# Kernel optimization log

Measured on AMD Instinct MI355X. Metric: run time of the kernel, lower is better.

## Reference

```python
import jax, jax.numpy as jnp
import numpy as np

B, T, I, H, L = 32, 1024, 1024, 1024, 3


def setup_inputs() -> dict:
    key = jax.random.key(0)
    ks = jax.random.split(key, 8)
    sc_in = 1.0 / np.sqrt(I)
    sc_h = 1.0 / np.sqrt(H)
    return {
        "x": jax.random.normal(ks[0], (B, T, I), dtype=jnp.float32),
        "s0": jnp.zeros((B, H), dtype=jnp.float32),
        "w_h": jax.random.normal(ks[1], (I, H), dtype=jnp.float32) * sc_in,
        "w_t": jax.random.normal(ks[2], (I, H), dtype=jnp.float32) * sc_in,
        "w_c": jax.random.normal(ks[3], (I, H), dtype=jnp.float32) * sc_in,
        "Rh": jax.random.normal(ks[4], (L, H, H), dtype=jnp.float32) * sc_h,
        "Rt": jax.random.normal(ks[5], (L, H, H), dtype=jnp.float32) * sc_h,
        "Rc": jax.random.normal(ks[6], (L, H, H), dtype=jnp.float32) * sc_h,
        "bh": jnp.zeros((L, H), dtype=jnp.float32),
        "bt": jnp.zeros((L, H), dtype=jnp.float32),
        "bc": jnp.zeros((L, H), dtype=jnp.float32),
    }


def reference(x, s0, w_h, w_t, w_c, Rh, Rt, Rc, bh, bt, bc):
    # x: [B, T, I]; s0: [B, H]. Dropout prob = 0 -> identity.
    num_layers = Rh.shape[0]

    def step(s, x_t):
        # Input projections only feed layer 0 (as in the torch code).
        whx = x_t @ w_h  # [B, H]
        wtx = x_t @ w_t
        wcx = x_t @ w_c
        for l in range(num_layers):
            h_in = (whx if l == 0 else 0.0) + s @ Rh[l].T + bh[l]
            t_in = (wtx if l == 0 else 0.0) + s @ Rt[l].T + bt[l]
            c_in = (wcx if l == 0 else 0.0) + s @ Rc[l].T + bc[l]
            h = jnp.tanh(h_in)
            t = jax.nn.sigmoid(t_in)
            c = jax.nn.sigmoid(c_in)
            s = h * t + s * c
        return s, s

    x_tbi = jnp.swapaxes(x, 0, 1)  # [T, B, I] for scan over time
    s_T, outs = jax.lax.scan(step, s0, x_tbi)
    return jnp.swapaxes(outs, 0, 1), s_T  # ([B, T, H], [B, H])
```

## Files before the change

### kernel.cpp

```cpp
#include <hip/hip_runtime.h>
#include <hip/hip_bf16.h>

static constexpr int Bb = 32;
static constexpr int Tt = 1024;
static constexpr int Ii = 1024;
static constexpr int Hh = 1024;
static constexpr int NWG = 256;

static constexpr int SLOT_E = Hh * Bb;
static constexpr int NSLOT  = 3 * Tt + 1;

typedef float f4 __attribute__((ext_vector_type(4)));

static constexpr int LDS_WORDS = 36 * 1024 + 2 * 1536;
static constexpr int LDS_BYTES = LDS_WORDS * 4;

static constexpr unsigned SENT32 = 0x7FC0DEADu;
static constexpr unsigned SENT16 = 0x7FC1u;

template <typename PT> __device__ __forceinline__ float pt_to_f(PT v);
template <> __device__ __forceinline__ float pt_to_f<float>(float v) { return v; }
template <> __device__ __forceinline__ float pt_to_f<__hip_bfloat16>(__hip_bfloat16 v) { return __bfloat162float(v); }

template <typename PT> __device__ __forceinline__ PT f_to_pt(float v);
template <> __device__ __forceinline__ float f_to_pt<float>(float v) { return v; }
template <> __device__ __forceinline__ __hip_bfloat16 f_to_pt<__hip_bfloat16>(float v) { return __float2bfloat16(v); }

#define BGLD(dst, p, lit) \
    asm volatile("global_load_dwordx4 %0, %1, off offset:" lit " sc0 sc1" : "=v"(dst) : "v"(p))
#define BG8(sv, p, a,b,c,d2,e,f,g2,h) \
    BGLD(sv[0],p,a); BGLD(sv[1],p,b); BGLD(sv[2],p,c); BGLD(sv[3],p,d2); \
    BGLD(sv[4],p,e); BGLD(sv[5],p,f); BGLD(sv[6],p,g2); BGLD(sv[7],p,h)
#define BGLD2(dst, p, lit) \
    asm volatile("global_load_dwordx2 %0, %1, off offset:" lit " sc0 sc1" : "=v"(dst) : "v"(p))
#define BG8x2(su, p, a,b,c,d2,e,f,g2,h) \
    BGLD2(su[0],p,a); BGLD2(su[1],p,b); BGLD2(su[2],p,c); BGLD2(su[3],p,d2); \
    BGLD2(su[4],p,e); BGLD2(su[5],p,f); BGLD2(su[6],p,g2); BGLD2(su[7],p,h)
#define VWAIT(n) do { asm volatile("s_waitcnt vmcnt(" #n ")" ::: "memory"); \
                      __builtin_amdgcn_sched_barrier(0); } while (0)

__device__ __forceinline__ int grp_ok32(const f4* sv) {
    int ok = 1;
#pragma unroll
    for (int i = 0; i < 8; ++i)
#pragma unroll
        for (int j = 0; j < 4; ++j)
            ok &= (__float_as_uint(sv[i][j]) != SENT32);
    return ok;
}
__device__ __forceinline__ int grp_ok16(const uint2* su) {
    int ok = 1;
#pragma unroll
    for (int i = 0; i < 8; ++i) {
        ok &= ((su[i].x & 0xFFFFu) != SENT16) & ((su[i].x >> 16) != SENT16);
        ok &= ((su[i].y & 0xFFFFu) != SENT16) & ((su[i].y >> 16) != SENT16);
    }
    return ok;
}

template <typename PT>
__global__ __launch_bounds__(256, 2) void proj_gemm(
    const float* __restrict__ X, const float* __restrict__ Wh,
    const float* __restrict__ Wt, const float* __restrict__ Wc,
    PT* __restrict__ P2)
{
    __shared__ float smem[4160];
    float* As = smem;
    float* Bs = smem + 1088;

    const int tid = threadIdx.x;
    const int tx = tid & 15, ty = tid >> 4;
    const int col0 = blockIdx.x * 64;
    const int t0 = blockIdx.y * 2;

    float acc[3][4][4];
#pragma unroll
    for (int g = 0; g < 3; ++g)
#pragma unroll
        for (int mm = 0; mm < 4; ++mm)
#pragma unroll
            for (int nn = 0; nn < 4; ++nn) acc[g][mm][nn] = 0.f;

    const int lm = tid >> 2, lk4 = (tid & 3) * 4;
    const float* aptr = X + ((size_t)(lm & 31) * Tt + (t0 + (lm >> 5))) * Ii + lk4;
    const int bk = tid >> 4, bn4 = (tid & 15) * 4;

    for (int k0 = 0; k0 < Ii; k0 += 16) {
        float4 av = *(const float4*)(aptr + k0);
        As[(lk4 + 0) * 68 + lm] = av.x;
        As[(lk4 + 1) * 68 + lm] = av.y;
        As[(lk4 + 2) * 68 + lm] = av.z;
        As[(lk4 + 3) * 68 + lm] = av.w;
        *(float4*)&Bs[0 * 1024 + bk * 64 + bn4] = *(const float4*)(Wh + (size_t)(k0 + bk) * Hh + col0 + bn4);
        *(float4*)&Bs[1 * 1024 + bk * 64 + bn4] = *(const float4*)(Wt + (size_t)(k0 + bk) * Hh + col0 + bn4);
        *(float4*)&Bs[2 * 1024 + bk * 64 + bn4] = *(const float4*)(Wc + (size_t)(k0 + bk) * Hh + col0 + bn4);
        __syncthreads();
#pragma unroll
        for (int k = 0; k < 16; ++k) {
            float4 a = *(const float4*)&As[k * 68 + ty * 4];
            float a_[4] = {a.x, a.y, a.z, a.w};
#pragma unroll
            for (int g = 0; g < 3; ++g) {
                float4 b = *(const float4*)&Bs[g * 1024 + k * 64 + tx * 4];
                float b_[4] = {b.x, b.y, b.z, b.w};
#pragma unroll
                for (int mm = 0; mm < 4; ++mm)
#pragma unroll
                    for (int nn = 0; nn < 4; ++nn)
                        acc[g][mm][nn] += a_[mm] * b_[nn];
            }
        }
        __syncthreads();
    }

    float* E = smem;
    const int b4 = (tid & 7) * 4;
#pragma unroll 1
    for (int g = 0; g < 3; ++g) {
        __syncthreads();
#pragma unroll
        for (int mm = 0; mm < 4; ++mm)
#pragma unroll
            for (int nn = 0; nn < 4; ++nn)
                E[(ty * 4 + mm) * 65 + tx * 4 + nn] = acc[g][mm][nn];
        __syncthreads();
        PT* dst = P2 + (size_t)g * Tt * Hh * Bb;
#pragma unroll
        for (int it = 0; it < 4; ++it) {
            const int line = (tid >> 3) + it * 32;
            const int tt = line >> 6, hh = line & 63;
            const float o0 = E[(tt * 32 + b4 + 0) * 65 + hh];
            const float o1 = E[(tt * 32 + b4 + 1) * 65 + hh];
            const float o2v = E[(tt * 32 + b4 + 2) * 65 + hh];
            const float o3 = E[(tt * 32 + b4 + 3) * 65 + hh];
            PT* d = dst + ((size_t)(t0 + tt) * Hh + col0 + hh) * Bb + b4;
            d[0] = f_to_pt<PT>(o0); d[1] = f_to_pt<PT>(o1);
            d[2] = f_to_pt<PT>(o2v); d[3] = f_to_pt<PT>(o3);
        }
    }
}

template <typename RT>
__global__ __launch_bounds__(256) void init_ring(const float* __restrict__ s0,
                                                 RT* __restrict__ ring)
{
    const size_t tid = (size_t)blockIdx.x * 256 + threadIdx.x;
    if (tid < (size_t)Bb * Hh) {
        const int b = (int)(tid >> 10), h = (int)(tid & 1023);
        ring[h * 32 + b] = f_to_pt<RT>(s0[tid]);
    }
    const unsigned sw = (sizeof(RT) == 4) ? SENT32 : ((SENT16 << 16) | SENT16);
    const uint4 pat = {sw, sw, sw, sw};
    uint4* base = (uint4*)(ring + SLOT_E);
    const size_t n16 = (size_t)(NSLOT - 1) * SLOT_E * sizeof(RT) / 16;
    const size_t stride = (size_t)gridDim.x * 256;
    for (size_t i = tid; i < n16; i += stride) base[i] = pat;
}

template <typename RT>
__global__ __launch_bounds__(256) void out_transpose(
    const RT* __restrict__ ring, float* __restrict__ out, float* __restrict__ sT)
{
    __shared__ float tile[128 * 33];
    const int tid = threadIdx.x;
    const int h0 = blockIdx.x * 128;
    const int t = blockIdx.y;
    const RT* src = ring + (size_t)(3 * t + 3) * SLOT_E + h0 * 32;
#pragma unroll
    for (int e = 0; e < 16; ++e) {
        const int idx = e * 256 + tid;
        tile[(idx >> 5) * 33 + (idx & 31)] = pt_to_f<RT>(src[idx]);
    }
    __syncthreads();
    const int hi = tid & 31, bq = tid >> 5;
#pragma unroll
    for (int e = 0; e < 4; ++e) {
        const int b = bq + e * 8;
        float4 v;
        v.x = tile[(hi * 4 + 0) * 33 + b];
        v.y = tile[(hi * 4 + 1) * 33 + b];
        v.z = tile[(hi * 4 + 2) * 33 + b];
        v.w = tile[(hi * 4 + 3) * 33 + b];
        *(float4*)(out + ((size_t)b * Tt + t) * Hh + h0 + hi * 4) = v;
        if (t == Tt - 1) *(float4*)(sT + (size_t)b * Hh + h0 + hi * 4) = v;
    }
}

template <typename PT, typename RT>
__global__ __launch_bounds__(256, 1) void rhn_recur(
    const float* __restrict__ Rh, const float* __restrict__ Rt,
    const float* __restrict__ Rc, const float* __restrict__ bh,
    const float* __restrict__ bt, const float* __restrict__ bc,
    const PT* __restrict__ P2, RT* __restrict__ ring)
{
    extern __shared__ float lds[];

    const int g = blockIdx.x;
    const int tid = threadIdx.x;

    {
        const int k4 = tid * 4;
        const int sk = k4 ^ (((k4 >> 5) & 7) << 2);
#pragma unroll 1
        for (int j = 0; j < 36; ++j) {
            const int l = j / 12;
            const int rem = j - l * 12;
            const int gt = rem >> 2;
            const int q = rem & 3;
            const int h = (q << 8) | g;
            const float* src = (gt == 0 ? Rh : (gt == 1 ? Rt : Rc)) + ((size_t)l * Hh + h) * Hh;
            *(float4*)&lds[(j << 10) | sk] = *(const float4*)(src + k4);
        }
    }
    __syncthreads();

    const int ks = tid >> 3;
    const int b0 = (tid & 7) << 2;
    const int q8 = ks & 7;
    const int wv = tid >> 6;
    const int ub = tid & 31;
    const int uqc = (tid >> 5) & 3;
    const int uhc = (uqc << 8) | g;

    int o2[8];
#pragma unroll
    for (int c = 0; c < 8; ++c) o2[c] = ((c ^ q8) << 2);

    float brh[3], brt[3], brc[3];
#pragma unroll
    for (int l = 0; l < 3; ++l) {
        brh[l] = bh[l * Hh + uhc];
        brt[l] = bt[l * Hh + uhc];
        brc[l] = bc[l * Hh + uhc];
    }

    float so_reg = pt_to_f<RT>(ring[uhc * 32 + ub]);

#pragma unroll 1
    for (int t = 0; t < Tt; ++t) {
#pragma unroll 1
        for (int l = 0; l < 3; ++l) {
            const int p = t * 3 + l;
            float* part = lds + 36 * 1024 + (p & 1) * 1536;

            float pv0 = 0.f, pv1 = 0.f, pv2 = 0.f;
            if (l == 0 && tid < 128) {
                const size_t pb = ((size_t)t * Hh + uhc) * Bb + ub;
                pv0 = pt_to_f<PT>(P2[pb]);
                pv1 = pt_to_f<PT>(P2[(size_t)Tt * Hh * Bb + pb]);
                pv2 = pt_to_f<PT>(P2[2 * (size_t)Tt * Hh * Bb + pb]);
            }

            const float* rp = lds + l * 12288 + (ks << 5);

            f4 accv[12];
#pragma unroll
            for (int jj = 0; jj < 12; ++jj) accv[jj] = (f4){0.f, 0.f, 0.f, 0.f};

            if constexpr (sizeof(RT) == 4) {
                const float* sA = (const float*)ring + (size_t)p * SLOT_E + (ks << 5) * 32 + b0;
                f4 sv0[8], sv1[8];
                BG8(sv0, sA, "0","128","256","384","512","640","768","896");
                BG8(sv1, sA, "1024","1152","1280","1408","1536","1664","1792","1920");
                VWAIT(8);
                while (!__all(grp_ok32(sv0))) {
                    __builtin_amdgcn_s_sleep(1);
                    BG8(sv0, sA, "0","128","256","384","512","640","768","896");
                    VWAIT(0);
                }
#pragma unroll
                for (int jj = 0; jj < 12; ++jj) {
                    const f4 r0 = *(const f4*)(rp + jj * 1024 + o2[0]);
                    const f4 r1 = *(const f4*)(rp + jj * 1024 + o2[1]);
                    f4 a = accv[jj];
                    a += sv0[0] * r0[0]; a += sv0[1] * r0[1]; a += sv0[2] * r0[2]; a += sv0[3] * r0[3];
                    a += sv0[4] * r1[0]; a += sv0[5] * r1[1]; a += sv0[6] * r1[2]; a += sv0[7] * r1[3];
                    accv[jj] = a;
                }
                BG8(sv0, sA, "2048","2176","2304","2432","2560","2688","2816","2944");
                VWAIT(8);
                while (!__all(grp_ok32(sv1))) {
                    __builtin_amdgcn_s_sleep(1);
                    BG8(sv1, sA, "1024","1152","1280","1408","1536","1664","1792","1920");
                    VWAIT(0);
                }
#pragma unroll
                for (int jj = 0; jj < 12; ++jj) {
                    const f4 r0 = *(const f4*)(rp + jj * 1024 + o2[2]);
                    const f4 r1 = *(const f4*)(rp + jj * 1024 + o2[3]);
                    f4 a = accv[jj];
                    a += sv1[0] * r0[0]; a += sv1[1] * r0[1]; a += sv1[2] * r0[2]; a += sv1[3] * r0[3];
                    a += sv1[4] * r1[0]; a += sv1[5] * r1[1]; a += sv1[6] * r1[2]; a += sv1[7] * r1[3];
                    accv[jj] = a;
                }
                BG8(sv1, sA, "3072","3200","3328","3456","3584","3712","3840","3968");
                VWAIT(8);
                while (!__all(grp_ok32(sv0))) {
                    __builtin_amdgcn_s_sleep(1);
                    BG8(sv0, sA, "2048","2176","2304","2432","2560","2688","2816","2944");
                    VWAIT(0);
                }
#pragma unroll
                for (int jj = 0; jj < 12; ++jj) {
                    const f4 r0 = *(const f4*)(rp + jj * 1024 + o2[4]);
                    const f4 r1 = *(const f4*)(rp + jj * 1024 + o2[5]);
                    f4 a = accv[jj];
                    a += sv0[0] * r0[0]; a += sv0[1] * r0[1]; a += sv0[2] * r0[2]; a += sv0[3] * r0[3];
                    a += sv0[4] * r1[0]; a += sv0[5] * r1[1]; a += sv0[6] * r1[2]; a += sv0[7] * r1[3];
                    accv[jj] = a;
                }
                VWAIT(0);
                while (!__all(grp_ok32(sv1))) {
                    __builtin_amdgcn_s_sleep(1);
                    BG8(sv1, sA, "3072","3200","3328","3456","3584","3712","3840","3968");
                    VWAIT(0);
                }
#pragma unroll
                for (int jj = 0; jj < 12; ++jj) {
                    const f4 r0 = *(const f4*)(rp + jj * 1024 + o2[6]);
                    const f4 r1 = *(const f4*)(rp + jj * 1024 + o2[7]);
                    f4 a = accv[jj];
                    a += sv1[0] * r0[0]; a += sv1[1] * r0[1]; a += sv1[2] * r0[2]; a += sv1[3] * r0[3];
                    a += sv1[4] * r1[0]; a += sv1[5] * r1[1]; a += sv1[6] * r1[2]; a += sv1[7] * r1[3];
                    accv[jj] = a;
                }
            } else {
                const __hip_bfloat16* sIn = (const __hip_bfloat16*)ring + (size_t)p * SLOT_E + (ks << 5) * 32 + b0;
#pragma unroll 1
                for (int blk = 0; blk < 4; ++blk) {
                    uint2 su[8];
                    const __hip_bfloat16* pb2 = sIn + (size_t)blk * 256;
                    BG8x2(su, pb2, "0","64","128","192","256","320","384","448");
                    VWAIT(0);
                    while (!__all(grp_ok16(su))) {
                        __builtin_amdgcn_s_sleep(1);
                        BG8x2(su, pb2, "0","64","128","192","256","320","384","448");
                        VWAIT(0);
                    }
                    f4 sv[8];
#pragma unroll
                    for (int i = 0; i < 8; ++i) {
                        sv[i][0] = __uint_as_float(su[i].x << 16);
                        sv[i][1] = __uint_as_float(su[i].x & 0xFFFF0000u);
                        sv[i][2] = __uint_as_float(su[i].y << 16);
                        sv[i][3] = __uint_as_float(su[i].y & 0xFFFF0000u);
                    }
#pragma unroll
                    for (int jj = 0; jj < 12; ++jj) {
                        const f4 r0 = *(const f4*)(rp + jj * 1024 + o2[blk * 2]);
                        const f4 r1 = *(const f4*)(rp + jj * 1024 + o2[blk * 2 + 1]);
                        f4 a = accv[jj];
                        a += sv[0] * r0[0]; a += sv[1] * r0[1]; a += sv[2] * r0[2]; a += sv[3] * r0[3];
                        a += sv[4] * r1[0]; a += sv[5] * r1[1]; a += sv[6] * r1[2]; a += sv[7] * r1[3];
                        accv[jj] = a;
                    }
                }
            }

#pragma unroll
            for (int jj = 0; jj < 12; ++jj) {
#pragma unroll
                for (int st = 8; st <= 32; st <<= 1) {
                    accv[jj][0] += __shfl_xor(accv[jj][0], st);
                    accv[jj][1] += __shfl_xor(accv[jj][1], st);
                    accv[jj][2] += __shfl_xor(accv[jj][2], st);
                    accv[jj][3] += __shfl_xor(accv[jj][3], st);
                }
            }
            f4 s1 = accv[0];
#pragma unroll
            for (int j2 = 1; j2 < 8; ++j2) if (q8 == j2) s1 = accv[j2];
            f4 s2 = accv[8];
#pragma unroll
            for (int j2 = 1; j2 < 4; ++j2) if (q8 == j2) s2 = accv[8 + j2];
            *(f4*)&part[(wv * 12 + q8) * 32 + b0] = s1;
            if (q8 < 4) *(f4*)&part[(wv * 12 + 8 + q8) * 32 + b0] = s2;
            __syncthreads();

            if (tid < 128) {
                float vals[3];
#pragma unroll
                for (int gt = 0; gt < 3; ++gt) {
                    const int jl = (gt << 2) + uqc;
                    vals[gt] = part[jl * 32 + ub] + part[(12 + jl) * 32 + ub]
                             + part[(24 + jl) * 32 + ub] + part[(36 + jl) * 32 + ub];
                }
                float bb0, bb1, bb2;
                if (l == 0)      { bb0 = brh[0]; bb1 = brt[0]; bb2 = brc[0]; }
                else if (l == 1) { bb0 = brh[1]; bb1 = brt[1]; bb2 = brc[1]; }
                else             { bb0 = brh[2]; bb1 = brt[2]; bb2 = brc[2]; }
                vals[0] += bb0; vals[1] += bb1; vals[2] += bb2;
                if (l == 0) { vals[0] += pv0; vals[1] += pv1; vals[2] += pv2; }
                const float hv = 1.f - 2.f / (1.f + __expf(2.f * vals[0]));
                const float tv = 1.f / (1.f + __expf(-vals[1]));
                const float cv = 1.f / (1.f + __expf(-vals[2]));
                const float sn = hv * tv + so_reg * cv;
                so_reg = sn;
                RT* wp = ring + (size_t)(p + 1) * SLOT_E + uhc * 32 + ub;
                if constexpr (sizeof(RT) == 4) {
                    __hip_atomic_store((float*)wp, sn, __ATOMIC_RELAXED, __HIP_MEMORY_SCOPE_AGENT);
                } else {
                    __hip_bfloat16 b16 = __float2bfloat16(sn);
                    __hip_atomic_store((unsigned short*)wp, *(unsigned short*)&b16,
                                       __ATOMIC_RELAXED, __HIP_MEMORY_SCOPE_AGENT);
                }
            }
        }
    }
}

extern "C" void kernel_launch(void* const* d_in, const int* in_sizes, int n_in,
                              void* d_out, int out_size, void* d_ws, size_t ws_size,
                              hipStream_t stream)
{
    (void)in_sizes; (void)n_in; (void)out_size;
    const float* x  = (const float*)d_in[0];
    const float* s0 = (const float*)d_in[1];
    const float* wh = (const float*)d_in[2];
    const float* wt = (const float*)d_in[3];
    const float* wc = (const float*)d_in[4];
    const float* Rh = (const float*)d_in[5];
    const float* Rt = (const float*)d_in[6];
    const float* Rc = (const float*)d_in[7];
    const float* bh = (const float*)d_in[8];
    const float* bt = (const float*)d_in[9];
    const float* bc = (const float*)d_in[10];

    float* out = (float*)d_out;
    float* sT  = out + (size_t)Bb * Tt * Hh;

    const size_t THB  = (size_t)Tt * Hh * Bb;
    const size_t p2f  = 3 * THB * 4, p2h = 3 * THB * 2;
    const size_t ringF = (size_t)NSLOT * SLOT_E * 4;
    const size_t ringH = (size_t)NSLOT * SLOT_E * 2;

    char* w = (char*)d_ws;

    if (ws_size >= p2f + ringF) {
        float* P2 = (float*)w;
        float* ring = (float*)(w + p2f);
        proj_gemm<float><<<dim3(16, 512), 256, 0, stream>>>(x, wh, wt, wc, P2);
        init_ring<float><<<2048, 256, 0, stream>>>(s0, ring);
        hipFuncSetAttribute(reinterpret_cast<const void*>(rhn_recur<float, float>),
                            hipFuncAttributeMaxDynamicSharedMemorySize, LDS_BYTES);
        void* args[] = {(void*)&Rh, (void*)&Rt, (void*)&Rc, (void*)&bh, (void*)&bt, (void*)&bc,
                        (void*)&P2, (void*)&ring};
        hipLaunchCooperativeKernel(reinterpret_cast<void*>(rhn_recur<float, float>),
                                   dim3(NWG), dim3(256), args, LDS_BYTES, stream);
        out_transpose<float><<<dim3(8, 1024), 256, 0, stream>>>(ring, out, sT);
    } else if (ws_size >= p2h + ringF) {
        __hip_bfloat16* P2 = (__hip_bfloat16*)w;
        float* ring = (float*)(w + p2h);
        proj_gemm<__hip_bfloat16><<<dim3(16, 512), 256, 0, stream>>>(x, wh, wt, wc, P2);
        init_ring<float><<<2048, 256, 0, stream>>>(s0, ring);
        hipFuncSetAttribute(reinterpret_cast<const void*>(rhn_recur<__hip_bfloat16, float>),
                            hipFuncAttributeMaxDynamicSharedMemorySize, LDS_BYTES);
        void* args[] = {(void*)&Rh, (void*)&Rt, (void*)&Rc, (void*)&bh, (void*)&bt, (void*)&bc,
                        (void*)&P2, (void*)&ring};
        hipLaunchCooperativeKernel(reinterpret_cast<void*>(rhn_recur<__hip_bfloat16, float>),
                                   dim3(NWG), dim3(256), args, LDS_BYTES, stream);
        out_transpose<float><<<dim3(8, 1024), 256, 0, stream>>>(ring, out, sT);
    } else {
        __hip_bfloat16* P2 = (__hip_bfloat16*)w;
        __hip_bfloat16* ring = (__hip_bfloat16*)(w + p2h);
        proj_gemm<__hip_bfloat16><<<dim3(16, 512), 256, 0, stream>>>(x, wh, wt, wc, P2);
        init_ring<__hip_bfloat16><<<2048, 256, 0, stream>>>(s0, ring);
        hipFuncSetAttribute(reinterpret_cast<const void*>(rhn_recur<__hip_bfloat16, __hip_bfloat16>),
                            hipFuncAttributeMaxDynamicSharedMemorySize, LDS_BYTES);
        void* args[] = {(void*)&Rh, (void*)&Rt, (void*)&Rc, (void*)&bh, (void*)&bt, (void*)&bc,
                        (void*)&P2, (void*)&ring};
        hipLaunchCooperativeKernel(reinterpret_cast<void*>(rhn_recur<__hip_bfloat16, __hip_bfloat16>),
                                   dim3(NWG), dim3(256), args, LDS_BYTES, stream);
        out_transpose<__hip_bfloat16><<<dim3(8, 1024), 256, 0, stream>>>(ring, out, sT);
    }
}
```

Baseline: 32.00 ms.

## Replace full-length sentinel ring with 16-slot tagged ring and history buffer

```diff
diff --git a/kernel.cpp b/kernel.cpp
--- a/kernel.cpp
+++ b/kernel.cpp
@@ -8,15 +8,12 @@
 static constexpr int NWG = 256;
 
 static constexpr int SLOT_E = Hh * Bb;
-static constexpr int NSLOT  = 3 * Tt + 1;
+static constexpr int NS     = 16;
 
 typedef float f4 __attribute__((ext_vector_type(4)));
 
 static constexpr int LDS_WORDS = 36 * 1024 + 2 * 1536;
 static constexpr int LDS_BYTES = LDS_WORDS * 4;
-
-static constexpr unsigned SENT32 = 0x7FC0DEADu;
-static constexpr unsigned SENT16 = 0x7FC1u;
 
 template <typename PT> __device__ __forceinline__ float pt_to_f(PT v);
 template <> __device__ __forceinline__ float pt_to_f<float>(float v) { return v; }
@@ -25,38 +22,40 @@
 template <typename PT> __device__ __forceinline__ PT f_to_pt(float v);
 template <> __device__ __forceinline__ float f_to_pt<float>(float v) { return v; }
 template <> __device__ __forceinline__ __hip_bfloat16 f_to_pt<__hip_bfloat16>(float v) { return __float2bfloat16(v); }
+
+__device__ __forceinline__ void backoff(int it) {
+    if (it < 2)      __builtin_amdgcn_s_sleep(1);
+    else if (it < 4) __builtin_amdgcn_s_sleep(2);
+    else if (it < 8) __builtin_amdgcn_s_sleep(4);
+    else             __builtin_amdgcn_s_sleep(8);
+}
 
 #define BGLD(dst, p, lit) \
     asm volatile("global_load_dwordx4 %0, %1, off offset:" lit " sc0 sc1" : "=v"(dst) : "v"(p))
 #define BG8(sv, p, a,b,c,d2,e,f,g2,h) \
     BGLD(sv[0],p,a); BGLD(sv[1],p,b); BGLD(sv[2],p,c); BGLD(sv[3],p,d2); \
     BGLD(sv[4],p,e); BGLD(sv[5],p,f); BGLD(sv[6],p,g2); BGLD(sv[7],p,h)
-#define BGLD2(dst, p, lit) \
-    asm volatile("global_load_dwordx2 %0, %1, off offset:" lit " sc0 sc1" : "=v"(dst) : "v"(p))
-#define BG8x2(su, p, a,b,c,d2,e,f,g2,h) \
-    BGLD2(su[0],p,a); BGLD2(su[1],p,b); BGLD2(su[2],p,c); BGLD2(su[3],p,d2); \
-    BGLD2(su[4],p,e); BGLD2(su[5],p,f); BGLD2(su[6],p,g2); BGLD2(su[7],p,h)
 #define VWAIT(n) do { asm volatile("s_waitcnt vmcnt(" #n ")" ::: "memory"); \
                       __builtin_amdgcn_sched_barrier(0); } while (0)
 
-__device__ __forceinline__ int grp_ok32(const f4* sv) {
+__device__ __forceinline__ int grp_tag32(const f4* sv, unsigned texp) {
     int ok = 1;
 #pragma unroll
     for (int i = 0; i < 8; ++i)
 #pragma unroll
         for (int j = 0; j < 4; ++j)
-            ok &= (__float_as_uint(sv[i][j]) != SENT32);
+            ok &= (int)((__float_as_uint(sv[i][j]) & 3u) == texp);
     return ok;
 }
-__device__ __forceinline__ int grp_ok16(const uint2* su) {
-    int ok = 1;
-#pragma unroll
-    for (int i = 0; i < 8; ++i) {
-        ok &= ((su[i].x & 0xFFFFu) != SENT16) & ((su[i].x >> 16) != SENT16);
-        ok &= ((su[i].y & 0xFFFFu) != SENT16) & ((su[i].y >> 16) != SENT16);
-    }
-    return ok;
-}
+
+#define RETRY32T(sv, texp, p, a,b,c,d2,e,f,g2,h) \
+    { int _it = 0; \
+      while (!__all(grp_tag32(sv, texp))) { \
+          if (_it) backoff(_it); \
+          ++_it; \
+          BG8(sv, p, a,b,c,d2,e,f,g2,h); \
+          VWAIT(0); \
+      } }
 
 template <typename PT>
 __global__ __launch_bounds__(256, 2) void proj_gemm(
@@ -140,36 +139,33 @@
     }
 }
 
-template <typename RT>
-__global__ __launch_bounds__(256) void init_ring(const float* __restrict__ s0,
-                                                 RT* __restrict__ ring)
+__global__ __launch_bounds__(256) void init_ring_s(const float* __restrict__ s0,
+                                                   float* __restrict__ ring)
 {
     const size_t tid = (size_t)blockIdx.x * 256 + threadIdx.x;
     if (tid < (size_t)Bb * Hh) {
         const int b = (int)(tid >> 10), h = (int)(tid & 1023);
-        ring[h * 32 + b] = f_to_pt<RT>(s0[tid]);
-    }
-    const unsigned sw = (sizeof(RT) == 4) ? SENT32 : ((SENT16 << 16) | SENT16);
-    const uint4 pat = {sw, sw, sw, sw};
+        ring[h * 32 + b] = __uint_as_float(__float_as_uint(s0[tid]) & ~3u);
+    }
+    const uint4 pat = {3u, 3u, 3u, 3u};
     uint4* base = (uint4*)(ring + SLOT_E);
-    const size_t n16 = (size_t)(NSLOT - 1) * SLOT_E * sizeof(RT) / 16;
+    const size_t n16 = (size_t)(NS - 1) * SLOT_E * 4 / 16;
     const size_t stride = (size_t)gridDim.x * 256;
     for (size_t i = tid; i < n16; i += stride) base[i] = pat;
 }
 
-template <typename RT>
-__global__ __launch_bounds__(256) void out_transpose(
-    const RT* __restrict__ ring, float* __restrict__ out, float* __restrict__ sT)
+__global__ __launch_bounds__(256) void out_transpose_hist(
+    const float* __restrict__ shist, float* __restrict__ out, float* __restrict__ sT)
 {
     __shared__ float tile[128 * 33];
     const int tid = threadIdx.x;
     const int h0 = blockIdx.x * 128;
     const int t = blockIdx.y;
-    const RT* src = ring + (size_t)(3 * t + 3) * SLOT_E + h0 * 32;
+    const float* src = shist + ((size_t)t * Hh + h0) * Bb;
 #pragma unroll
     for (int e = 0; e < 16; ++e) {
         const int idx = e * 256 + tid;
-        tile[(idx >> 5) * 33 + (idx & 31)] = pt_to_f<RT>(src[idx]);
+        tile[(idx >> 5) * 33 + (idx & 31)] = src[idx];
     }
     __syncthreads();
     const int hi = tid & 31, bq = tid >> 5;
@@ -186,12 +182,13 @@
     }
 }
 
-template <typename PT, typename RT>
+template <typename PT>
 __global__ __launch_bounds__(256, 1) void rhn_recur(
     const float* __restrict__ Rh, const float* __restrict__ Rt,
     const float* __restrict__ Rc, const float* __restrict__ bh,
     const float* __restrict__ bt, const float* __restrict__ bc,
-    const PT* __restrict__ P2, RT* __restrict__ ring)
+    const PT* __restrict__ P2, float* __restrict__ ring,
+    float* __restrict__ shist, const float* __restrict__ s0in)
 {
     extern __shared__ float lds[];
 
@@ -234,13 +231,17 @@
         brc[l] = bc[l * Hh + uhc];
     }
 
-    float so_reg = pt_to_f<RT>(ring[uhc * 32 + ub]);
+    float so_reg = (tid < 128) ? s0in[(size_t)ub * Hh + uhc] : 0.f;
 
 #pragma unroll 1
     for (int t = 0; t < Tt; ++t) {
 #pragma unroll 1
         for (int l = 0; l < 3; ++l) {
             const int p = t * 3 + l;
+            const int slr = p & (NS - 1);
+            const unsigned texp = (unsigned)((p >> 4) & 3);
+            const int slw = (p + 1) & (NS - 1);
+            const unsigned twr = (unsigned)(((p + 1) >> 4) & 3);
             float* part = lds + 36 * 1024 + (p & 1) * 1536;
 
             float pv0 = 0.f, pv1 = 0.f, pv2 = 0.f;
@@ -257,104 +258,55 @@
 #pragma unroll
             for (int jj = 0; jj < 12; ++jj) accv[jj] = (f4){0.f, 0.f, 0.f, 0.f};
 
-            if constexpr (sizeof(RT) == 4) {
-                const float* sA = (const float*)ring + (size_t)p * SLOT_E + (ks << 5) * 32 + b0;
-                f4 sv0[8], sv1[8];
-                BG8(sv0, sA, "0","128","256","384","512","640","768","896");
-                BG8(sv1, sA, "1024","1152","1280","1408","1536","1664","1792","1920");
-                VWAIT(8);
-                while (!__all(grp_ok32(sv0))) {
-                    __builtin_amdgcn_s_sleep(1);
-                    BG8(sv0, sA, "0","128","256","384","512","640","768","896");
-                    VWAIT(0);
-                }
-#pragma unroll
-                for (int jj = 0; jj < 12; ++jj) {
-                    const f4 r0 = *(const f4*)(rp + jj * 1024 + o2[0]);
-                    const f4 r1 = *(const f4*)(rp + jj * 1024 + o2[1]);
-                    f4 a = accv[jj];
-                    a += sv0[0] * r0[0]; a += sv0[1] * r0[1]; a += sv0[2] * r0[2]; a += sv0[3] * r0[3];
-                    a += sv0[4] * r1[0]; a += sv0[5] * r1[1]; a += sv0[6] * r1[2]; a += sv0[7] * r1[3];
-                    accv[jj] = a;
-                }
-                BG8(sv0, sA, "2048","2176","2304","2432","2560","2688","2816","2944");
-                VWAIT(8);
-                while (!__all(grp_ok32(sv1))) {
-                    __builtin_amdgcn_s_sleep(1);
-                    BG8(sv1, sA, "1024","1152","1280","1408","1536","1664","1792","1920");
-                    VWAIT(0);
-                }
-#pragma unroll
-                for (int jj = 0; jj < 12; ++jj) {
-                    const f4 r0 = *(const f4*)(rp + jj * 1024 + o2[2]);
-                    const f4 r1 = *(const f4*)(rp + jj * 1024 + o2[3]);
-                    f4 a = accv[jj];
-                    a += sv1[0] * r0[0]; a += sv1[1] * r0[1]; a += sv1[2] * r0[2]; a += sv1[3] * r0[3];
-                    a += sv1[4] * r1[0]; a += sv1[5] * r1[1]; a += sv1[6] * r1[2]; a += sv1[7] * r1[3];
-                    accv[jj] = a;
-                }
-                BG8(sv1, sA, "3072","3200","3328","3456","3584","3712","3840","3968");
-                VWAIT(8);
-                while (!__all(grp_ok32(sv0))) {
-                    __builtin_amdgcn_s_sleep(1);
-                    BG8(sv0, sA, "2048","2176","2304","2432","2560","2688","2816","2944");
-                    VWAIT(0);
-                }
-#pragma unroll
-                for (int jj = 0; jj < 12; ++jj) {
-                    const f4 r0 = *(const f4*)(rp + jj * 1024 + o2[4]);
-                    const f4 r1 = *(const f4*)(rp + jj * 1024 + o2[5]);
-                    f4 a = accv[jj];
-                    a += sv0[0] * r0[0]; a += sv0[1] * r0[1]; a += sv0[2] * r0[2]; a += sv0[3] * r0[3];
-                    a += sv0[4] * r1[0]; a += sv0[5] * r1[1]; a += sv0[6] * r1[2]; a += sv0[7] * r1[3];
-                    accv[jj] = a;
-                }
-                VWAIT(0);
-                while (!__all(grp_ok32(sv1))) {
-                    __builtin_amdgcn_s_sleep(1);
-                    BG8(sv1, sA, "3072","3200","3328","3456","3584","3712","3840","3968");
-                    VWAIT(0);
-                }
-#pragma unroll
-                for (int jj = 0; jj < 12; ++jj) {
-                    const f4 r0 = *(const f4*)(rp + jj * 1024 + o2[6]);
-                    const f4 r1 = *(const f4*)(rp + jj * 1024 + o2[7]);
-                    f4 a = accv[jj];
-                    a += sv1[0] * r0[0]; a += sv1[1] * r0[1]; a += sv1[2] * r0[2]; a += sv1[3] * r0[3];
-                    a += sv1[4] * r1[0]; a += sv1[5] * r1[1]; a += sv1[6] * r1[2]; a += sv1[7] * r1[3];
-                    accv[jj] = a;
-                }
-            } else {
-                const __hip_bfloat16* sIn = (const __hip_bfloat16*)ring + (size_t)p * SLOT_E + (ks << 5) * 32 + b0;
-#pragma unroll 1
-                for (int blk = 0; blk < 4; ++blk) {
-                    uint2 su[8];
-                    const __hip_bfloat16* pb2 = sIn + (size_t)blk * 256;
-                    BG8x2(su, pb2, "0","64","128","192","256","320","384","448");
-                    VWAIT(0);
-                    while (!__all(grp_ok16(su))) {
-                        __builtin_amdgcn_s_sleep(1);
-                        BG8x2(su, pb2, "0","64","128","192","256","320","384","448");
-                        VWAIT(0);
-                    }
-                    f4 sv[8];
-#pragma unroll
-                    for (int i = 0; i < 8; ++i) {
-                        sv[i][0] = __uint_as_float(su[i].x << 16);
-                        sv[i][1] = __uint_as_float(su[i].x & 0xFFFF0000u);
-                        sv[i][2] = __uint_as_float(su[i].y << 16);
-                        sv[i][3] = __uint_as_float(su[i].y & 0xFFFF0000u);
-                    }
-#pragma unroll
-                    for (int jj = 0; jj < 12; ++jj) {
-                        const f4 r0 = *(const f4*)(rp + jj * 1024 + o2[blk * 2]);
-                        const f4 r1 = *(const f4*)(rp + jj * 1024 + o2[blk * 2 + 1]);
-                        f4 a = accv[jj];
-                        a += sv[0] * r0[0]; a += sv[1] * r0[1]; a += sv[2] * r0[2]; a += sv[3] * r0[3];
-                        a += sv[4] * r1[0]; a += sv[5] * r1[1]; a += sv[6] * r1[2]; a += sv[7] * r1[3];
-                        accv[jj] = a;
-                    }
-                }
+            const float* sA = ring + (size_t)slr * SLOT_E + (ks << 5) * 32 + b0;
+            f4 sv0[8], sv1[8];
+            BG8(sv0, sA, "0","128","256","384","512","640","768","896");
+            BG8(sv1, sA, "1024","1152","1280","1408","1536","1664","1792","1920");
+            VWAIT(8);
+            RETRY32T(sv0, texp, sA, "0","128","256","384","512","640","768","896");
+#pragma unroll
+            for (int jj = 0; jj < 12; ++jj) {
+                const f4 r0 = *(const f4*)(rp + jj * 1024 + o2[0]);
+                const f4 r1 = *(const f4*)(rp + jj * 1024 + o2[1]);
+                f4 a = accv[jj];
+                a += sv0[0] * r0[0]; a += sv0[1] * r0[1]; a += sv0[2] * r0[2]; a += sv0[3] * r0[3];
+                a += sv0[4] * r1[0]; a += sv0[5] * r1[1]; a += sv0[6] * r1[2]; a += sv0[7] * r1[3];
+                accv[jj] = a;
+            }
+            BG8(sv0, sA, "2048","2176","2304","2432","2560","2688","2816","2944");
+            VWAIT(8);
+            RETRY32T(sv1, texp, sA, "1024","1152","1280","1408","1536","1664","1792","1920");
+#pragma unroll
+            for (int jj = 0; jj < 12; ++jj) {
+                const f4 r0 = *(const f4*)(rp + jj * 1024 + o2[2]);
+                const f4 r1 = *(const f4*)(rp + jj * 1024 + o2[3]);
+                f4 a = accv[jj];
+                a += sv1[0] * r0[0]; a += sv1[1] * r0[1]; a += sv1[2] * r0[2]; a += sv1[3] * r0[3];
+                a += sv1[4] * r1[0]; a += sv1[5] * r1[1]; a += sv1[6] * r1[2]; a += sv1[7] * r1[3];
+                accv[jj] = a;
+            }
+            BG8(sv1, sA, "3072","3200","3328","3456","3584","3712","3840","3968");
+            VWAIT(8);
+            RETRY32T(sv0, texp, sA, "2048","2176","2304","2432","2560","2688","2816","2944");
+#pragma unroll
+            for (int jj = 0; jj < 12; ++jj) {
+                const f4 r0 = *(const f4*)(rp + jj * 1024 + o2[4]);
+                const f4 r1 = *(const f4*)(rp + jj * 1024 + o2[5]);
+                f4 a = accv[jj];
+                a += sv0[0] * r0[0]; a += sv0[1] * r0[1]; a += sv0[2] * r0[2]; a += sv0[3] * r0[3];
+                a += sv0[4] * r1[0]; a += sv0[5] * r1[1]; a += sv0[6] * r1[2]; a += sv0[7] * r1[3];
+                accv[jj] = a;
+            }
+            VWAIT(0);
+            RETRY32T(sv1, texp, sA, "3072","3200","3328","3456","3584","3712","3840","3968");
+#pragma unroll
+            for (int jj = 0; jj < 12; ++jj) {
+                const f4 r0 = *(const f4*)(rp + jj * 1024 + o2[6]);
+                const f4 r1 = *(const f4*)(rp + jj * 1024 + o2[7]);
+                f4 a = accv[jj];
+                a += sv1[0] * r0[0]; a += sv1[1] * r0[1]; a += sv1[2] * r0[2]; a += sv1[3] * r0[3];
+                a += sv1[4] * r1[0]; a += sv1[5] * r1[1]; a += sv1[6] * r1[2]; a += sv1[7] * r1[3];
+                accv[jj] = a;
             }
 
 #pragma unroll
@@ -396,16 +348,31 @@
                 const float cv = 1.f / (1.f + __expf(-vals[2]));
                 const float sn = hv * tv + so_reg * cv;
                 so_reg = sn;
-                RT* wp = ring + (size_t)(p + 1) * SLOT_E + uhc * 32 + ub;
-                if constexpr (sizeof(RT) == 4) {
-                    __hip_atomic_store((float*)wp, sn, __ATOMIC_RELAXED, __HIP_MEMORY_SCOPE_AGENT);
-                } else {
-                    __hip_bfloat16 b16 = __float2bfloat16(sn);
-                    __hip_atomic_store((unsigned short*)wp, *(unsigned short*)&b16,
-                                       __ATOMIC_RELAXED, __HIP_MEMORY_SCOPE_AGENT);
-                }
+                const unsigned bits = (__float_as_uint(sn) & ~3u) | twr;
+                __hip_atomic_store((unsigned*)(ring + (size_t)slw * SLOT_E + uhc * 32 + ub),
+                                   bits, __ATOMIC_RELAXED, __HIP_MEMORY_SCOPE_AGENT);
+                if (l == 2)
+                    shist[((size_t)t * Hh + uhc) * Bb + ub] = sn;
             }
         }
+    }
+}
+
+template <typename PT>
+static void launch_recur(const float* Rh, const float* Rt, const float* Rc,
+                         const float* bh, const float* bt, const float* bc,
+                         const PT* P2, float* ring, float* shist,
+                         const float* s0, hipStream_t stream)
+{
+    (void)hipFuncSetAttribute(reinterpret_cast<const void*>(rhn_recur<PT>),
+                              hipFuncAttributeMaxDynamicSharedMemorySize, LDS_BYTES);
+    void* args[] = {(void*)&Rh, (void*)&Rt, (void*)&Rc, (void*)&bh, (void*)&bt, (void*)&bc,
+                    (void*)&P2, (void*)&ring, (void*)&shist, (void*)&s0};
+    hipError_t e = hipLaunchCooperativeKernel(reinterpret_cast<void*>(rhn_recur<PT>),
+                                              dim3(NWG), dim3(256), args, LDS_BYTES, stream);
+    if (e != hipSuccess) {
+        rhn_recur<PT><<<dim3(NWG), dim3(256), LDS_BYTES, stream>>>(
+            Rh, Rt, Rc, bh, bt, bc, P2, ring, shist, s0);
     }
 }
 
@@ -429,48 +396,28 @@
     float* out = (float*)d_out;
     float* sT  = out + (size_t)Bb * Tt * Hh;
 
-    const size_t THB  = (size_t)Tt * Hh * Bb;
-    const size_t p2f  = 3 * THB * 4, p2h = 3 * THB * 2;
-    const size_t ringF = (size_t)NSLOT * SLOT_E * 4;
-    const size_t ringH = (size_t)NSLOT * SLOT_E * 2;
+    const size_t THB   = (size_t)Tt * Hh * Bb;
+    const size_t p2f   = 3 * THB * 4, p2h = 3 * THB * 2;
+    const size_t ringS = (size_t)NS * SLOT_E * 4;
+    const size_t shF   = THB * 4;
 
     char* w = (char*)d_ws;
 
-    if (ws_size >= p2f + ringF) {
+    if (ws_size >= p2f + ringS + shF + 4096) {
         float* P2 = (float*)w;
         float* ring = (float*)(w + p2f);
+        float* shist = (float*)(w + p2f + ringS);
         proj_gemm<float><<<dim3(16, 512), 256, 0, stream>>>(x, wh, wt, wc, P2);
-        init_ring<float><<<2048, 256, 0, stream>>>(s0, ring);
-        hipFuncSetAttribute(reinterpret_cast<const void*>(rhn_recur<float, float>),
-                            hipFuncAttributeMaxDynamicSharedMemorySize, LDS_BYTES);
-        void* args[] = {(void*)&Rh, (void*)&Rt, (void*)&Rc, (void*)&bh, (void*)&bt, (void*)&bc,
-                        (void*)&P2, (void*)&ring};
-        hipLaunchCooperativeKernel(reinterpret_cast<void*>(rhn_recur<float, float>),
-                                   dim3(NWG), dim3(256), args, LDS_BYTES, stream);
-        out_transpose<float><<<dim3(8, 1024), 256, 0, stream>>>(ring, out, sT);
-    } else if (ws_size >= p2h + ringF) {
+        init_ring_s<<<128, 256, 0, stream>>>(s0, ring);
+        launch_recur<float>(Rh, Rt, Rc, bh, bt, bc, P2, ring, shist, s0, stream);
+        out_transpose_hist<<<dim3(8, 1024), 256, 0, stream>>>(shist, out, sT);
+    } else {
         __hip_bfloat16* P2 = (__hip_bfloat16*)w;
         float* ring = (float*)(w + p2h);
+        float* shist = (float*)(w + p2h + ringS);
         proj_gemm<__hip_bfloat16><<<dim3(16, 512), 256, 0, stream>>>(x, wh, wt, wc, P2);
-        init_ring<float><<<2048, 256, 0, stream>>>(s0, ring);
-        hipFuncSetAttribute(reinterpret_cast<const void*>(rhn_recur<__hip_bfloat16, float>),
-                            hipFuncAttributeMaxDynamicSharedMemorySize, LDS_BYTES);
-        void* args[] = {(void*)&Rh, (void*)&Rt, (void*)&Rc, (void*)&bh, (void*)&bt, (void*)&bc,
-                        (void*)&P2, (void*)&ring};
-        hipLaunchCooperativeKernel(reinterpret_cast<void*>(rhn_recur<__hip_bfloat16, float>),
-                                   dim3(NWG), dim3(256), args, LDS_BYTES, stream);
-        out_transpose<float><<<dim3(8, 1024), 256, 0, stream>>>(ring, out, sT);
-    } else {
-        __hip_bfloat16* P2 = (__hip_bfloat16*)w;
-        __hip_bfloat16* ring = (__hip_bfloat16*)(w + p2h);
-        proj_gemm<__hip_bfloat16><<<dim3(16, 512), 256, 0, stream>>>(x, wh, wt, wc, P2);
-        init_ring<__hip_bfloat16><<<2048, 256, 0, stream>>>(s0, ring);
-        hipFuncSetAttribute(reinterpret_cast<const void*>(rhn_recur<__hip_bfloat16, __hip_bfloat16>),
-                            hipFuncAttributeMaxDynamicSharedMemorySize, LDS_BYTES);
-        void* args[] = {(void*)&Rh, (void*)&Rt, (void*)&Rc, (void*)&bh, (void*)&bt, (void*)&bc,
-                        (void*)&P2, (void*)&ring};
-        hipLaunchCooperativeKernel(reinterpret_cast<void*>(rhn_recur<__hip_bfloat16, __hip_bfloat16>),
-                                   dim3(NWG), dim3(256), args, LDS_BYTES, stream);
-        out_transpose<__hip_bfloat16><<<dim3(8, 1024), 256, 0, stream>>>(ring, out, sT);
-    }
-}
+        init_ring_s<<<128, 256, 0, stream>>>(s0, ring);
+        launch_recur<__hip_bfloat16>(Rh, Rt, Rc, bh, bt, bc, P2, ring, shist, s0, stream);
+        out_transpose_hist<<<dim3(8, 1024), 256, 0, stream>>>(shist, out, sT);
+    }
+}
```

Result: no change. 32.54 ms (+1.7%).
